# Kernel optimization log

Measured on AMD Instinct MI355X. Metric: run time of the kernel, lower is better.

The kernel has to match this reference:

```python
import jax, jax.numpy as jnp
import numpy as np

B, P, C = 32, 8732, 21
TOP_K = 200
CONF_THRESH = 0.01
NMS_THRESH = 0.45
VAR0, VAR1 = 0.1, 0.2  # VOC PRIOR_BOX VARIANCE


def setup_inputs() -> dict:
    key = jax.random.key(0)
    k1, k2, k3 = jax.random.split(key, 3)
    loc_data = jax.random.normal(k1, (B, P, 4), jnp.float32)
    conf_data = jax.random.uniform(k2, (B, P, C), jnp.float32)
    prior_data = jax.random.uniform(k3, (P, 4), jnp.float32)
    return {"loc_data": loc_data, "conf_data": conf_data, "prior_data": prior_data}


def _decode(loc, priors):
    # priors are (cx, cy, w, h); returns (x1, y1, x2, y2)
    cxcy = priors[:, :2] + loc[:, :2] * VAR0 * priors[:, 2:]
    wh = priors[:, 2:] * jnp.exp(loc[:, 2:] * VAR1)
    x1y1 = cxcy - wh * 0.5
    return jnp.concatenate([x1y1, x1y1 + wh], axis=1)  # [P,4]


def _nms_class(boxes, scores):
    # boxes [P,4], scores [P] -> [TOP_K,5] rows of (score, x1, y1, x2, y2)
    s = jnp.where(scores > CONF_THRESH, scores, -1.0)
    top_s, idx = jax.lax.top_k(s, TOP_K)          # descending scores
    b = boxes[idx]                                 # [K,4]
    valid = top_s > CONF_THRESH
    x1, y1, x2, y2 = b[:, 0], b[:, 1], b[:, 2], b[:, 3]
    area = (x2 - x1) * (y2 - y1)
    # pairwise intersection / IoU [K,K]
    xx1 = jnp.maximum(x1[:, None], x1[None, :])
    yy1 = jnp.maximum(y1[:, None], y1[None, :])
    xx2 = jnp.minimum(x2[:, None], x2[None, :])
    yy2 = jnp.minimum(y2[:, None], y2[None, :])
    inter = jnp.clip(xx2 - xx1, 0.0) * jnp.clip(yy2 - yy1, 0.0)
    union = area[:, None] + area[None, :] - inter
    iou = inter / union
    ar = jnp.arange(TOP_K)

    def step(carry, j):
        kept, suppressed = carry
        is_kept = valid[j] & ~suppressed[j]
        kept = kept.at[j].set(is_kept)
        suppressed = suppressed | (is_kept & (iou[j] > NMS_THRESH) & (ar > j))
        return (kept, suppressed), None

    (kept, _), _ = jax.lax.scan(
        step, (jnp.zeros(TOP_K, bool), jnp.zeros(TOP_K, bool)), ar)
    # compact kept rows to the front (matches output[i, cl, :count] = ...)
    pos = jnp.cumsum(kept) - 1
    safe = jnp.where(kept, pos, TOP_K)
    rows = jnp.concatenate([top_s[:, None], b], axis=1)  # [K,5]
    out = jnp.zeros((TOP_K + 1, 5), rows.dtype).at[safe].set(rows)[:TOP_K]
    return out


def reference(loc_data, conf_data, prior_data):
    def per_image(loc, conf):
        boxes = _decode(loc, prior_data)           # [P,4]
        return jax.vmap(lambda s: _nms_class(boxes, s), in_axes=1)(conf)  # [C,K,5]

    out = jax.vmap(per_image)(loc_data, conf_data)  # [B,C,K,5]
    return out.at[:, 0].set(0.0)  # class 0 (background) is skipped in original
```

## Files before the change

kernel.cpp:

```cpp
#include <hip/hip_runtime.h>
#include <stdint.h>

#define B_ 32
#define P_ 8732
#define PPAD 8736
#define C_ 21
#define TOPK 200
#define CONF_T 0.01f
#define NMS_T 0.45f
#define NCH2 35
#define NT 512
#define KV4 5

__device__ __forceinline__ uint32_t f2s(float f) {
    uint32_t u = __float_as_uint(f);
    return (u & 0x80000000u) ? ~u : (u | 0x80000000u);
}
__device__ __forceinline__ float s2f(uint32_t s) {
    uint32_t b = (s & 0x80000000u) ? (s & 0x7FFFFFFFu) : ~s;
    return __uint_as_float(b);
}

__global__ __launch_bounds__(256) void transpose_keys(const float* __restrict__ conf,
                                                      uint32_t* __restrict__ keys) {
    const int b = blockIdx.x / NCH2;
    const int ch = blockIdx.x % NCH2;
    const int p0 = ch * 256;
    const int n = min(256, P_ - p0);
    const int tid = threadIdx.x;
    __shared__ float tile[256 * C_];
    const float* src = conf + ((size_t)b * P_ + p0) * C_;
    const int tot = n * C_;
    for (int i = tid; i < tot; i += 256) tile[i] = src[i];
    __syncthreads();
    uint32_t* dst = keys + (size_t)b * C_ * PPAD + p0;
    if (tid < n) {
        #pragma unroll
        for (int c = 0; c < C_; ++c) {
            float v = tile[tid * C_ + c];
            v = (v > CONF_T) ? v : -1.0f;
            dst[(size_t)c * PPAD + tid] = f2s(v);
        }
    }
    if (ch == NCH2 - 1 && tid >= n && tid < n + (PPAD - P_)) {
        #pragma unroll
        for (int c = 0; c < C_; ++c) dst[(size_t)c * PPAD + tid] = 0u;
    }
}

template<bool RAW>
__global__ __launch_bounds__(NT, 6) void detect_kernel(
    const float* __restrict__ loc, const float* __restrict__ prior,
    const uint32_t* __restrict__ keys, const float* __restrict__ conf,
    float* __restrict__ out)
{
    const int task = blockIdx.x;
    const int b = task / C_;
    const int c = task % C_;
    const int tid = threadIdx.x;
    const int lane = tid & 63;
    float* outp = out + (size_t)task * TOPK * 5;

    if (c == 0) {
        for (int e = tid; e < TOPK * 5; e += NT) outp[e] = 0.0f;
        return;
    }

    __shared__ uint32_t hist[512];
    __shared__ uint64_t cand[256];
    __shared__ float4 bbox[TOPK];
    __shared__ float bar[TOPK], bs[TOPK];
    __shared__ unsigned long long msk[TOPK * 4];
    __shared__ unsigned long long vmask[4];
    __shared__ int order[TOPK];
    __shared__ int s_cnt, s_nk, s_flags;
    __shared__ uint32_t s_pref, s_want;

    uint4 kv[KV4];
    if (!RAW) {
        const uint4* kp = (const uint4*)(keys + (size_t)task * PPAD);
        #pragma unroll
        for (int r = 0; r < KV4; ++r) {
            int q = tid + r * NT;
            kv[r] = (q < PPAD / 4) ? kp[q] : make_uint4(0u, 0u, 0u, 0u);
        }
    } else {
        const float* sp = conf + (size_t)b * P_ * C_ + c;
        #pragma unroll
        for (int r = 0; r < KV4; ++r) {
            uint32_t uu[4];
            #pragma unroll
            for (int c4 = 0; c4 < 4; ++c4) {
                int p = (tid + r * NT) * 4 + c4;
                if (p < P_) {
                    float v = sp[(size_t)p * C_];
                    v = (v > CONF_T) ? v : -1.0f;
                    uu[c4] = f2s(v);
                } else uu[c4] = 0u;
            }
            kv[r] = make_uint4(uu[0], uu[1], uu[2], uu[3]);
        }
    }

    if (tid == 0) s_cnt = 0;
    if (tid < 512) hist[tid] = 0;
    for (int i2 = tid; i2 < TOPK * 4; i2 += NT) msk[i2] = 0ull;
    __syncthreads();

    uint32_t pref = 0, want = TOPK;
    for (int level = 3; level >= 0; --level) {
        const int shift = level * 8;
        uint32_t* H = hist + ((((3 - level) & 1)) << 8);
        if (level <= 1) {
            if (tid < 256) H[tid] = 0;
            __syncthreads();
        }
        if (level == 3) {
            auto agg = [&](uint32_t u) {
                uint32_t bin = u >> 24;
                unsigned long long rem = __ballot(1);
                while (rem) {
                    int src = __ffsll(rem) - 1;
                    uint32_t bref = __shfl(bin, src);
                    unsigned long long same = __ballot(bin == bref) & rem;
                    if (lane == src) atomicAdd(&H[bref], (uint32_t)__popcll(same));
                    rem &= ~same;
                }
            };
            #pragma unroll
            for (int r = 0; r < KV4; ++r) {
                agg(kv[r].x); agg(kv[r].y); agg(kv[r].z); agg(kv[r].w);
            }
        } else {
            const uint32_t himask = 0xFFFFFFFFu << (shift + 8);
            auto one = [&](uint32_t u) {
                if ((u & himask) == pref) atomicAdd(&H[(u >> shift) & 0xFFu], 1u);
            };
            #pragma unroll
            for (int r = 0; r < KV4; ++r) {
                one(kv[r].x); one(kv[r].y); one(kv[r].z); one(kv[r].w);
            }
        }
        __syncthreads();
        if (tid < 64) {
            uint4 bb = ((const uint4*)H)[tid];
            uint32_t s = bb.x + bb.y + bb.z + bb.w;
            uint32_t I = s;
            #pragma unroll
            for (int d = 1; d < 64; d <<= 1) {
                uint32_t t2 = __shfl_down(I, d);
                if (lane + d < 64) I += t2;
            }
            const uint32_t above = I - s;
            const uint32_t e3 = above,      i3 = above + bb.w;
            const uint32_t e2 = i3,         i2 = i3 + bb.z;
            const uint32_t e1 = i2,         i1 = i2 + bb.y;
            const uint32_t e0 = i1,         i0 = i1 + bb.x;
            const uint32_t base = (uint32_t)TOPK - want;
            if (i3 >= want && e3 < want) {
                s_pref = pref | ((uint32_t)(4 * tid + 3) << shift);
                s_want = want - e3; s_flags = (base + i3 <= 256);
            }
            if (i2 >= want && e2 < want) {
                s_pref = pref | ((uint32_t)(4 * tid + 2) << shift);
                s_want = want - e2; s_flags = (base + i2 <= 256);
            }
            if (i1 >= want && e1 < want) {
                s_pref = pref | ((uint32_t)(4 * tid + 1) << shift);
                s_want = want - e1; s_flags = (base + i1 <= 256);
            }
            if (i0 >= want && e0 < want) {
                s_pref = pref | ((uint32_t)(4 * tid + 0) << shift);
                s_want = want - e0; s_flags = (base + i0 <= 256);
            }
        }
        __syncthreads();
        pref = s_pref; want = s_want;
        if (s_flags) break;
    }
    const uint32_t vthr = pref;

    #pragma unroll
    for (int r = 0; r < KV4; ++r) {
        const int pb = (tid + r * NT) * 4;
        uint32_t uu[4] = {kv[r].x, kv[r].y, kv[r].z, kv[r].w};
        #pragma unroll
        for (int c4 = 0; c4 < 4; ++c4) {
            uint32_t u = uu[c4];
            if (u >= vthr) {
                int pos = atomicAdd(&s_cnt, 1);
                if (pos < 256) cand[pos] = ((uint64_t)u << 32) | (uint32_t)(~(uint32_t)(pb + c4));
            }
        }
    }
    __syncthreads();
    if (tid < 256 && tid >= s_cnt) cand[tid] = 0ull;
    __syncthreads();

    uint64_t v = (tid < 256) ? cand[tid] : 0ull;
    for (int kk = 2; kk <= 256; kk <<= 1) {
        for (int j = kk >> 1; j > 0; j >>= 1) {
            if (j >= 64) {
                __syncthreads();
                if (tid < 256) cand[tid] = v;
                __syncthreads();
                if (tid < 256) {
                    uint64_t pv = cand[tid ^ j];
                    bool keepmax = (((tid & j) == 0) == ((tid & kk) == 0));
                    v = keepmax ? (v > pv ? v : pv) : (v < pv ? v : pv);
                }
            } else if (tid < 256) {
                uint64_t pv = __shfl_xor(v, j);
                bool keepmax = (((tid & j) == 0) == ((tid & kk) == 0));
                v = keepmax ? (v > pv ? v : pv) : (v < pv ? v : pv);
            }
        }
    }

    float my_sc = -1.0f;
    if (tid < TOPK) {
        uint32_t su = (uint32_t)(v >> 32);
        int p = (int)(~(uint32_t)v);
        my_sc = s2f(su);
        const float4 l4 = *(const float4*)(loc + ((size_t)b * P_ + p) * 4);
        const float4 pr = *(const float4*)(prior + (size_t)p * 4);
        float cx = __fadd_rn(pr.x, __fmul_rn(__fmul_rn(l4.x, 0.1f), pr.z));
        float cy = __fadd_rn(pr.y, __fmul_rn(__fmul_rn(l4.y, 0.1f), pr.w));
        float ew = (float)exp((double)__fmul_rn(l4.z, 0.2f));
        float eh = (float)exp((double)__fmul_rn(l4.w, 0.2f));
        float w  = __fmul_rn(pr.z, ew);
        float h  = __fmul_rn(pr.w, eh);
        float x1 = __fsub_rn(cx, __fmul_rn(w, 0.5f));
        float y1 = __fsub_rn(cy, __fmul_rn(h, 0.5f));
        float x2 = __fadd_rn(x1, w);
        float y2 = __fadd_rn(y1, h);
        bs[tid] = my_sc;
        bbox[tid] = make_float4(x1, y1, x2, y2);
        bar[tid] = __fmul_rn(__fsub_rn(x2, x1), __fsub_rn(y2, y1));
    }
    {
        unsigned long long bm = __ballot(tid < TOPK && my_sc > CONF_T);
        if (lane == 0 && tid < 256) vmask[tid >> 6] = bm;
    }
    __syncthreads();

    if (tid < 500) {
        const int rp = tid / 5;
        const int s  = tid - rp * 5;
        #pragma unroll
        for (int pass = 0; pass < 2; ++pass) {
            const int j  = pass ? (199 - rp) : rp;
            const int i0 = pass ? (200 - rp + s) : (rp + 1 + s);
            const float4 bj = bbox[j];
            const float  aj = bar[j];
            for (int i = i0; i < TOPK; i += 5) {
                const float4 bi = bbox[i];
                float xx1 = fmaxf(bj.x, bi.x);
                float yy1 = fmaxf(bj.y, bi.y);
                float xx2 = fminf(bj.z, bi.z);
                float yy2 = fminf(bj.w, bi.w);
                float dx = fmaxf(__fsub_rn(xx2, xx1), 0.0f);
                float dy = fmaxf(__fsub_rn(yy2, yy1), 0.0f);
                float inter = __fmul_rn(dx, dy);
                if (inter > 0.0f) {
                    float uni = __fsub_rn(__fadd_rn(aj, bar[i]), inter);
                    float t45 = __fmul_rn(NMS_T, uni);
                    float mar = __fmul_rn(t45, 1e-6f);
                    bool sup;
                    if (inter > __fadd_rn(t45, mar)) sup = true;
                    else if (inter < __fsub_rn(t45, mar)) sup = false;
                    else sup = (inter / uni > NMS_T);
                    if (sup) atomicOr(&msk[j * 4 + (i >> 6)], 1ull << (i & 63));
                }
            }
        }
    }
    __syncthreads();

    if (tid < 64) {
        const int L = tid;
        auto or_reduce = [&](unsigned long long x) {
            #pragma unroll
            for (int d = 1; d < 64; d <<= 1) x |= __shfl_xor(x, d);
            return x;
        };
        unsigned long long s1 = 0, s2 = 0, s3 = 0;
        int nk = 0;
        #pragma unroll
        for (int w = 0; w < 4; ++w) {
            const int j = (w << 6) | L;
            unsigned long long r0 = 0, r1 = 0, r2 = 0, r3 = 0;
            if (j < TOPK) {
                const unsigned long long* mr = &msk[j * 4];
                r0 = mr[0]; r1 = mr[1]; r2 = mr[2]; r3 = mr[3];
            }
            const unsigned long long rself = (w == 0) ? r0 : (w == 1) ? r1
                                           : (w == 2) ? r2 : r3;
            unsigned long long sw = (w == 0) ? 0ull : (w == 1) ? s1
                                  : (w == 2) ? s2 : s3;
            unsigned long long alive = vmask[w] & ~sw;
            unsigned long long pm = 0;
            while (alive) {
                int jl = __ffsll(alive) - 1;
                if (L == 0) order[nk] = (w << 6) | jl;
                ++nk;
                sw |= __shfl(rself, jl);
                pm |= (1ull << jl);
                alive &= ~(sw | (1ull << jl));
            }
            if (pm) {
                const bool picked = (pm >> L) & 1ull;
                if (w == 0) {
                    s1 |= or_reduce(picked ? r1 : 0ull);
                    s2 |= or_reduce(picked ? r2 : 0ull);
                    s3 |= or_reduce(picked ? r3 : 0ull);
                } else if (w == 1) {
                    s2 |= or_reduce(picked ? r2 : 0ull);
                    s3 |= or_reduce(picked ? r3 : 0ull);
                } else if (w == 2) {
                    s3 |= or_reduce(picked ? r3 : 0ull);
                }
            }
        }
        if (L == 0) s_nk = nk;
    }
    __syncthreads();

    const int nk = s_nk;
    for (int e = tid; e < TOPK * 5; e += NT) {
        int r = e / 5;
        int f = e - r * 5;
        float val = 0.0f;
        if (r < nk) {
            int j = order[r];
            float4 bb = bbox[j];
            val = (f == 0) ? bs[j] : (f == 1) ? bb.x : (f == 2) ? bb.y
                : (f == 3) ? bb.z : bb.w;
        }
        outp[e] = val;
    }
}

extern "C" void kernel_launch(void* const* d_in, const int* in_sizes, int n_in,
                              void* d_out, int out_size, void* d_ws, size_t ws_size,
                              hipStream_t stream) {
    const float* loc   = (const float*)d_in[0];
    const float* conf  = (const float*)d_in[1];
    const float* prior = (const float*)d_in[2];
    float* out = (float*)d_out;

    const size_t need = (size_t)B_ * C_ * PPAD * sizeof(uint32_t);
    if (ws_size >= need) {
        uint32_t* keys = (uint32_t*)d_ws;
        transpose_keys<<<B_ * NCH2, 256, 0, stream>>>(conf, keys);
        detect_kernel<false><<<B_ * C_, NT, 0, stream>>>(loc, prior, keys, conf, out);
    } else {
        detect_kernel<true><<<B_ * C_, NT, 0, stream>>>(loc, prior, nullptr, conf, out);
    }
}
```

Measured before the change: 136.3 us.

## Build top-byte radix histograms in transpose kernel, skip first pass in detect

The transpose kernel now computes the level-3 (top 8 bits) radix histogram for each (image, class) with wave-aggregated global atomics while it writes the keys. The detect kernel reads that histogram instead of running its own first histogram pass, which saves a pass over 8.7k keys per block and some shared-memory atomic work. In exchange it adds a memset launch, global atomics in the transpose kernel, and a dependency on extra workspace. The background class is also skipped in the transpose, and the NMS pair index start is rewritten to an equivalent form.

Result: slower. 161.7 us (+18.6%).

```diff
diff --git a/kernel.cpp b/kernel.cpp
--- a/kernel.cpp
+++ b/kernel.cpp
@@ -11,6 +11,7 @@
 #define NCH2 35
 #define NT 512
 #define KV4 5
+#define NTASK (B_ * C_)
 
 __device__ __forceinline__ uint32_t f2s(float f) {
     uint32_t u = __float_as_uint(f);
@@ -22,29 +23,46 @@
 }
 
 __global__ __launch_bounds__(256) void transpose_keys(const float* __restrict__ conf,
-                                                      uint32_t* __restrict__ keys) {
+                                                      uint32_t* __restrict__ keys,
+                                                      uint32_t* __restrict__ ghist) {
     const int b = blockIdx.x / NCH2;
     const int ch = blockIdx.x % NCH2;
     const int p0 = ch * 256;
     const int n = min(256, P_ - p0);
     const int tid = threadIdx.x;
+    const int lane = tid & 63;
     __shared__ float tile[256 * C_];
     const float* src = conf + ((size_t)b * P_ + p0) * C_;
     const int tot = n * C_;
     for (int i = tid; i < tot; i += 256) tile[i] = src[i];
     __syncthreads();
     uint32_t* dst = keys + (size_t)b * C_ * PPAD + p0;
-    if (tid < n) {
-        #pragma unroll
-        for (int c = 0; c < C_; ++c) {
+    #pragma unroll
+    for (int c = 1; c < C_; ++c) {
+        uint32_t key = 0;
+        const bool act = tid < n;
+        if (act) {
             float v = tile[tid * C_ + c];
             v = (v > CONF_T) ? v : -1.0f;
-            dst[(size_t)c * PPAD + tid] = f2s(v);
+            key = f2s(v);
+            dst[(size_t)c * PPAD + tid] = key;
+        }
+        if (act) {
+            uint32_t* gh = ghist + ((size_t)(b * C_ + c) << 8);
+            uint32_t bin = key >> 24;
+            unsigned long long rem = __ballot(1);
+            while (rem) {
+                int s = __ffsll(rem) - 1;
+                uint32_t bref = __shfl(bin, s);
+                unsigned long long same = __ballot(bin == bref) & rem;
+                if (lane == s) atomicAdd(&gh[bref], (uint32_t)__popcll(same));
+                rem &= ~same;
+            }
         }
     }
     if (ch == NCH2 - 1 && tid >= n && tid < n + (PPAD - P_)) {
         #pragma unroll
-        for (int c = 0; c < C_; ++c) dst[(size_t)c * PPAD + tid] = 0u;
+        for (int c = 1; c < C_; ++c) dst[(size_t)c * PPAD + tid] = 0u;
     }
 }
 
@@ -52,7 +70,7 @@
 __global__ __launch_bounds__(NT, 6) void detect_kernel(
     const float* __restrict__ loc, const float* __restrict__ prior,
     const uint32_t* __restrict__ keys, const float* __restrict__ conf,
-    float* __restrict__ out)
+    const uint32_t* __restrict__ ghist, float* __restrict__ out)
 {
     const int task = blockIdx.x;
     const int b = task / C_;
@@ -105,33 +123,76 @@
     if (tid == 0) s_cnt = 0;
     if (tid < 512) hist[tid] = 0;
     for (int i2 = tid; i2 < TOPK * 4; i2 += NT) msk[i2] = 0ull;
-    __syncthreads();
+
+    auto scan_pick = [&](uint4 bb, int shift, uint32_t pref_c, uint32_t want_c) {
+        uint32_t s = bb.x + bb.y + bb.z + bb.w;
+        uint32_t I = s;
+        #pragma unroll
+        for (int d = 1; d < 64; d <<= 1) {
+            uint32_t t2 = __shfl_down(I, d);
+            if (lane + d < 64) I += t2;
+        }
+        const uint32_t above = I - s;
+        const uint32_t e3 = above,      i3 = above + bb.w;
+        const uint32_t e2 = i3,         i2 = i3 + bb.z;
+        const uint32_t e1 = i2,         i1 = i2 + bb.y;
+        const uint32_t e0 = i1,         i0 = i1 + bb.x;
+        const uint32_t base = (uint32_t)TOPK - want_c;
+        if (i3 >= want_c && e3 < want_c) {
+            s_pref = pref_c | ((uint32_t)(4 * lane + 3) << shift);
+            s_want = want_c - e3; s_flags = (base + i3 <= 256);
+        }
+        if (i2 >= want_c && e2 < want_c) {
+            s_pref = pref_c | ((uint32_t)(4 * lane + 2) << shift);
+            s_want = want_c - e2; s_flags = (base + i2 <= 256);
+        }
+        if (i1 >= want_c && e1 < want_c) {
+            s_pref = pref_c | ((uint32_t)(4 * lane + 1) << shift);
+            s_want = want_c - e1; s_flags = (base + i1 <= 256);
+        }
+        if (i0 >= want_c && e0 < want_c) {
+            s_pref = pref_c | ((uint32_t)(4 * lane + 0) << shift);
+            s_want = want_c - e0; s_flags = (base + i0 <= 256);
+        }
+    };
 
     uint32_t pref = 0, want = TOPK;
     for (int level = 3; level >= 0; --level) {
         const int shift = level * 8;
         uint32_t* H = hist + ((((3 - level) & 1)) << 8);
-        if (level <= 1) {
-            if (tid < 256) H[tid] = 0;
+        if (level == 3) {
+            if (!RAW) {
+                if (tid < 64) {
+                    const uint4* gh = (const uint4*)(ghist + ((size_t)task << 8));
+                    scan_pick(gh[lane], 24, 0u, TOPK);
+                }
+                __syncthreads();
+            } else {
+                __syncthreads();
+                auto agg = [&](uint32_t u) {
+                    uint32_t bin = u >> 24;
+                    unsigned long long rem = __ballot(1);
+                    while (rem) {
+                        int src = __ffsll(rem) - 1;
+                        uint32_t bref = __shfl(bin, src);
+                        unsigned long long same = __ballot(bin == bref) & rem;
+                        if (lane == src) atomicAdd(&H[bref], (uint32_t)__popcll(same));
+                        rem &= ~same;
+                    }
+                };
+                #pragma unroll
+                for (int r = 0; r < KV4; ++r) {
+                    agg(kv[r].x); agg(kv[r].y); agg(kv[r].z); agg(kv[r].w);
+                }
+                __syncthreads();
+                if (tid < 64) scan_pick(((const uint4*)H)[lane], 24, 0u, TOPK);
+                __syncthreads();
+            }
+        } else {
+            if (level <= 1) {
+                if (tid < 256) H[tid] = 0;
+            }
             __syncthreads();
-        }
-        if (level == 3) {
-            auto agg = [&](uint32_t u) {
-                uint32_t bin = u >> 24;
-                unsigned long long rem = __ballot(1);
-                while (rem) {
-                    int src = __ffsll(rem) - 1;
-                    uint32_t bref = __shfl(bin, src);
-                    unsigned long long same = __ballot(bin == bref) & rem;
-                    if (lane == src) atomicAdd(&H[bref], (uint32_t)__popcll(same));
-                    rem &= ~same;
-                }
-            };
-            #pragma unroll
-            for (int r = 0; r < KV4; ++r) {
-                agg(kv[r].x); agg(kv[r].y); agg(kv[r].z); agg(kv[r].w);
-            }
-        } else {
             const uint32_t himask = 0xFFFFFFFFu << (shift + 8);
             auto one = [&](uint32_t u) {
                 if ((u & himask) == pref) atomicAdd(&H[(u >> shift) & 0xFFu], 1u);
@@ -140,41 +201,10 @@
             for (int r = 0; r < KV4; ++r) {
                 one(kv[r].x); one(kv[r].y); one(kv[r].z); one(kv[r].w);
             }
-        }
-        __syncthreads();
-        if (tid < 64) {
-            uint4 bb = ((const uint4*)H)[tid];
-            uint32_t s = bb.x + bb.y + bb.z + bb.w;
-            uint32_t I = s;
-            #pragma unroll
-            for (int d = 1; d < 64; d <<= 1) {
-                uint32_t t2 = __shfl_down(I, d);
-                if (lane + d < 64) I += t2;
-            }
-            const uint32_t above = I - s;
-            const uint32_t e3 = above,      i3 = above + bb.w;
-            const uint32_t e2 = i3,         i2 = i3 + bb.z;
-            const uint32_t e1 = i2,         i1 = i2 + bb.y;
-            const uint32_t e0 = i1,         i0 = i1 + bb.x;
-            const uint32_t base = (uint32_t)TOPK - want;
-            if (i3 >= want && e3 < want) {
-                s_pref = pref | ((uint32_t)(4 * tid + 3) << shift);
-                s_want = want - e3; s_flags = (base + i3 <= 256);
-            }
-            if (i2 >= want && e2 < want) {
-                s_pref = pref | ((uint32_t)(4 * tid + 2) << shift);
-                s_want = want - e2; s_flags = (base + i2 <= 256);
-            }
-            if (i1 >= want && e1 < want) {
-                s_pref = pref | ((uint32_t)(4 * tid + 1) << shift);
-                s_want = want - e1; s_flags = (base + i1 <= 256);
-            }
-            if (i0 >= want && e0 < want) {
-                s_pref = pref | ((uint32_t)(4 * tid + 0) << shift);
-                s_want = want - e0; s_flags = (base + i0 <= 256);
-            }
-        }
-        __syncthreads();
+            __syncthreads();
+            if (tid < 64) scan_pick(((const uint4*)H)[lane], shift, pref, want);
+            __syncthreads();
+        }
         pref = s_pref; want = s_want;
         if (s_flags) break;
     }
@@ -250,7 +280,7 @@
         #pragma unroll
         for (int pass = 0; pass < 2; ++pass) {
             const int j  = pass ? (199 - rp) : rp;
-            const int i0 = pass ? (200 - rp + s) : (rp + 1 + s);
+            const int i0 = j + 1 + s;
             const float4 bj = bbox[j];
             const float  aj = bar[j];
             for (int i = i0; i < TOPK; i += 5) {
@@ -349,12 +379,15 @@
     const float* prior = (const float*)d_in[2];
     float* out = (float*)d_out;
 
-    const size_t need = (size_t)B_ * C_ * PPAD * sizeof(uint32_t);
-    if (ws_size >= need) {
-        uint32_t* keys = (uint32_t*)d_ws;
-        transpose_keys<<<B_ * NCH2, 256, 0, stream>>>(conf, keys);
-        detect_kernel<false><<<B_ * C_, NT, 0, stream>>>(loc, prior, keys, conf, out);
+    const size_t keys_bytes = (size_t)B_ * C_ * PPAD * sizeof(uint32_t);
+    const size_t hist_bytes = (size_t)NTASK * 256 * sizeof(uint32_t);
+    if (ws_size >= keys_bytes + hist_bytes) {
+        uint32_t* keys  = (uint32_t*)d_ws;
+        uint32_t* ghist = (uint32_t*)((char*)d_ws + keys_bytes);
+        hipMemsetAsync(ghist, 0, hist_bytes, stream);
+        transpose_keys<<<B_ * NCH2, 256, 0, stream>>>(conf, keys, ghist);
+        detect_kernel<false><<<B_ * C_, NT, 0, stream>>>(loc, prior, keys, conf, ghist, out);
     } else {
-        detect_kernel<true><<<B_ * C_, NT, 0, stream>>>(loc, prior, nullptr, conf, out);
-    }
-}
+        detect_kernel<true><<<B_ * C_, NT, 0, stream>>>(loc, prior, nullptr, conf, nullptr, out);
+    }
+}
```

## Replace radix-histogram top-k select with interpolation search on score threshold

Applied to the files above, without the earlier changes.

Replaces the four-level shared-memory radix histogram, which found the top-200 cutoff key, with an iterative threshold search. Each step counts the keys at or above a candidate threshold using a register compare, a wave shuffle reduction and one atomic per wave. The next threshold is interpolated from the count, assuming scores are roughly uniform, with a fallback to bisection. This removes the per-element LDS atomics and histogram scans, but the number of iterations now depends on the score distribution. The pairwise-IoU start index is rewritten into an equivalent simpler form.

Result: faster. 125.8 us (-7.7%).

```diff
diff --git a/kernel.cpp b/kernel.cpp
--- a/kernel.cpp
+++ b/kernel.cpp
@@ -6,6 +6,7 @@
 #define PPAD 8736
 #define C_ 21
 #define TOPK 200
+#define TGT 228
 #define CONF_T 0.01f
 #define NMS_T 0.45f
 #define NCH2 35
@@ -66,15 +67,14 @@
         return;
     }
 
-    __shared__ uint32_t hist[512];
     __shared__ uint64_t cand[256];
     __shared__ float4 bbox[TOPK];
     __shared__ float bar[TOPK], bs[TOPK];
     __shared__ unsigned long long msk[TOPK * 4];
     __shared__ unsigned long long vmask[4];
     __shared__ int order[TOPK];
-    __shared__ int s_cnt, s_nk, s_flags;
-    __shared__ uint32_t s_pref, s_want;
+    __shared__ int s_cnt, s_nk;
+    __shared__ int s_c2[2];
 
     uint4 kv[KV4];
     if (!RAW) {
@@ -103,82 +103,40 @@
     }
 
     if (tid == 0) s_cnt = 0;
-    if (tid < 512) hist[tid] = 0;
+    if (tid < 2) s_c2[tid] = 0;
     for (int i2 = tid; i2 < TOPK * 4; i2 += NT) msk[i2] = 0ull;
     __syncthreads();
 
-    uint32_t pref = 0, want = TOPK;
-    for (int level = 3; level >= 0; --level) {
-        const int shift = level * 8;
-        uint32_t* H = hist + ((((3 - level) & 1)) << 8);
-        if (level <= 1) {
-            if (tid < 256) H[tid] = 0;
-            __syncthreads();
-        }
-        if (level == 3) {
-            auto agg = [&](uint32_t u) {
-                uint32_t bin = u >> 24;
-                unsigned long long rem = __ballot(1);
-                while (rem) {
-                    int src = __ffsll(rem) - 1;
-                    uint32_t bref = __shfl(bin, src);
-                    unsigned long long same = __ballot(bin == bref) & rem;
-                    if (lane == src) atomicAdd(&H[bref], (uint32_t)__popcll(same));
-                    rem &= ~same;
-                }
-            };
-            #pragma unroll
-            for (int r = 0; r < KV4; ++r) {
-                agg(kv[r].x); agg(kv[r].y); agg(kv[r].z); agg(kv[r].w);
-            }
-        } else {
-            const uint32_t himask = 0xFFFFFFFFu << (shift + 8);
-            auto one = [&](uint32_t u) {
-                if ((u & himask) == pref) atomicAdd(&H[(u >> shift) & 0xFFu], 1u);
-            };
-            #pragma unroll
-            for (int r = 0; r < KV4; ++r) {
-                one(kv[r].x); one(kv[r].y); one(kv[r].z); one(kv[r].w);
-            }
-        }
+    uint32_t lo = 0u, hi = 0xFFFFFFFFu;
+    uint32_t t = f2s(1.0f - (float)TGT / (float)P_);
+    uint32_t vthr = 0u;
+    for (int it = 0; ; ++it) {
+        const int slot = it & 1;
+        int my = 0;
+        #pragma unroll
+        for (int r = 0; r < KV4; ++r)
+            my += (kv[r].x >= t) + (kv[r].y >= t) + (kv[r].z >= t) + (kv[r].w >= t);
+        #pragma unroll
+        for (int d = 1; d < 64; d <<= 1) my += __shfl_down(my, d);
+        if (lane == 0) atomicAdd(&s_c2[slot], my);
         __syncthreads();
-        if (tid < 64) {
-            uint4 bb = ((const uint4*)H)[tid];
-            uint32_t s = bb.x + bb.y + bb.z + bb.w;
-            uint32_t I = s;
-            #pragma unroll
-            for (int d = 1; d < 64; d <<= 1) {
-                uint32_t t2 = __shfl_down(I, d);
-                if (lane + d < 64) I += t2;
-            }
-            const uint32_t above = I - s;
-            const uint32_t e3 = above,      i3 = above + bb.w;
-            const uint32_t e2 = i3,         i2 = i3 + bb.z;
-            const uint32_t e1 = i2,         i1 = i2 + bb.y;
-            const uint32_t e0 = i1,         i0 = i1 + bb.x;
-            const uint32_t base = (uint32_t)TOPK - want;
-            if (i3 >= want && e3 < want) {
-                s_pref = pref | ((uint32_t)(4 * tid + 3) << shift);
-                s_want = want - e3; s_flags = (base + i3 <= 256);
-            }
-            if (i2 >= want && e2 < want) {
-                s_pref = pref | ((uint32_t)(4 * tid + 2) << shift);
-                s_want = want - e2; s_flags = (base + i2 <= 256);
-            }
-            if (i1 >= want && e1 < want) {
-                s_pref = pref | ((uint32_t)(4 * tid + 1) << shift);
-                s_want = want - e1; s_flags = (base + i1 <= 256);
-            }
-            if (i0 >= want && e0 < want) {
-                s_pref = pref | ((uint32_t)(4 * tid + 0) << shift);
-                s_want = want - e0; s_flags = (base + i0 <= 256);
-            }
-        }
+        const int cnt = s_c2[slot];
         __syncthreads();
-        pref = s_pref; want = s_want;
-        if (s_flags) break;
-    }
-    const uint32_t vthr = pref;
+        if (tid == 0) s_c2[slot] = 0;
+        if (cnt >= TOPK && cnt <= 256) { vthr = t; break; }
+        if (cnt > 256) lo = t; else hi = t;
+        if (hi - lo <= 1) { vthr = lo; break; }
+        uint32_t tn = 0;
+        bool bis = (it >= 8) || (cnt == 0);
+        if (!bis) {
+            const float sc = s2f(t);
+            const float sn = 1.0f - (1.0f - sc) * (float)TGT / (float)cnt;
+            tn = f2s(sn);
+            if (!(tn > lo && tn < hi)) bis = true;
+        }
+        if (bis) tn = lo + ((hi - lo) >> 1);
+        t = tn;
+    }
 
     #pragma unroll
     for (int r = 0; r < KV4; ++r) {
@@ -250,7 +208,7 @@
         #pragma unroll
         for (int pass = 0; pass < 2; ++pass) {
             const int j  = pass ? (199 - rp) : rp;
-            const int i0 = pass ? (200 - rp + s) : (rp + 1 + s);
+            const int i0 = j + 1 + s;
             const float4 bj = bbox[j];
             const float  aj = bar[j];
             for (int i = i0; i < TOPK; i += 5) {
```
